# Kernel optimization log

Measured on AMD Instinct MI355X. Metric: run time of the kernel, lower is better.

The kernel has to match this reference:

```python
import jax, jax.numpy as jnp
import numpy as np

H, DH = 8, 32          # heads, per-head dim
C = H * DH             # channels = 256
N = 20000              # nodes
E = 160000             # edges per relation
L = 4                  # layers
R = 2                  # edge types


def setup_inputs() -> dict:
    key = jax.random.key(0)
    ks = jax.random.split(key, 8)
    return {
        "x": jax.random.normal(ks[0], (N, C), jnp.float32),
        "ei0": jax.random.randint(ks[1], (2, E), 0, N, jnp.int32),
        "ei1": jax.random.randint(ks[2], (2, E), 0, N, jnp.int32),
        "kqv_w": jax.random.normal(ks[3], (L, C, 3 * C), jnp.float32) * 0.05,
        "kqv_b": jnp.zeros((L, 3 * C), jnp.float32),
        "out_w": jax.random.normal(ks[4], (L, C, C), jnp.float32) * 0.05,
        "out_b": jnp.zeros((L, C), jnp.float32),
        "skip": jnp.ones((L,), jnp.float32),
        "krel": jax.random.normal(ks[5], (L, R, H, DH, DH), jnp.float32) * 0.1,
        "vrel": jax.random.normal(ks[6], (L, R, H, DH, DH), jnp.float32) * 0.1,
        "prel": jnp.ones((L, R, H), jnp.float32),
        "ln_g": jnp.ones((L - 1, C), jnp.float32),
        "ln_b": jnp.zeros((L - 1, C), jnp.float32),
    }


def _segment_softmax(logits, seg, n):
    m = jax.ops.segment_max(logits, seg, num_segments=n)
    m = jnp.where(jnp.isfinite(m), m, 0.0)  # empty segments -> avoid -inf
    e = jnp.exp(logits - m[seg])
    s = jax.ops.segment_sum(e, seg, num_segments=n)
    return e / jnp.maximum(s[seg], 1e-16)


def _hgt_conv(x, edge_list, kqv_w, kqv_b, out_w, out_b, skip, krel, vrel, prel):
    n = x.shape[0]
    kqv = x @ kqv_w + kqv_b                       # [N, 3C]
    k, q, v = jnp.split(kqv, 3, axis=1)
    k = k.reshape(n, H, DH)
    q = q.reshape(n, H, DH)
    v = v.reshape(n, H, DH)
    logits, msgs, dsts = [], [], []
    for r, ei in enumerate(edge_list):            # loop over fixed small relation set
        src, dst = ei[0], ei[1]
        k_e = jnp.einsum('ehd,hdf->ehf', k[src], krel[r])   # relation-specific keys
        v_e = jnp.einsum('ehd,hdf->ehf', v[src], vrel[r])   # relation-specific values
        a = (q[dst] * k_e).sum(-1) * prel[r] / np.sqrt(DH)  # [E, H]
        logits.append(a)
        msgs.append(v_e)
        dsts.append(dst)
    logits = jnp.concatenate(logits, 0)
    msgs = jnp.concatenate(msgs, 0)
    dst = jnp.concatenate(dsts, 0)
    # softmax per destination node over ALL incoming edge types jointly (PyG HGTConv)
    alpha = _segment_softmax(logits, dst, n)      # [Etot, H]
    agg = jax.ops.segment_sum(msgs * alpha[:, :, None], dst, num_segments=n)
    agg = agg.reshape(n, C)
    a_out = jax.nn.gelu(agg, approximate=False) @ out_w + out_b
    s = jax.nn.sigmoid(skip)                      # skip applies: out dim == in dim
    return s * a_out + (1.0 - s) * x


def _layer_norm(h, g, b, eps=1e-5):
    mu = h.mean(-1, keepdims=True)
    var = ((h - mu) ** 2).mean(-1, keepdims=True)
    return (h - mu) * jax.lax.rsqrt(var + eps) * g + b


def reference(x, ei0, ei1, kqv_w, kqv_b, out_w, out_b, skip, krel, vrel, prel, ln_g, ln_b):
    edge_list = [ei0, ei1]
    h = x
    for i in range(L):
        h = _hgt_conv(h, edge_list, kqv_w[i], kqv_b[i], out_w[i], out_b[i],
                      skip[i], krel[i], vrel[i], prel[i])
        if i < L - 1:
            h = jax.nn.relu(h)
            h = _layer_norm(h, ln_g[i], ln_b[i])
            # dropout: identity in eval mode (p irrelevant at inference)
    return h
```

## Files before the change

kernel.cpp:

```cpp
#include <hip/hip_runtime.h>
#include <math.h>

#define NN 20000
#define NPAD 20096
#define CC 256
#define HH 8
#define EE 160000
#define TE 320000
#define KVSTRIDE 512
#define APAN ((size_t)NPAD*32)
#define BPAN 40960
#define OPAN 8192

typedef unsigned short u16;
typedef unsigned char u8;
typedef __attribute__((ext_vector_type(8))) short bf16x8;
typedef __attribute__((ext_vector_type(4))) float f32x4;
typedef __attribute__((ext_vector_type(2))) float f32x2;

__device__ __forceinline__ float gelu_exact(float x){
    return 0.5f*x*(1.0f+erff(x*0.7071067811865476f));
}
__device__ __forceinline__ u16 f2bf(float f){
    unsigned u = __float_as_uint(f);
    unsigned r = (u + 0x7fffu + ((u >> 16) & 1u)) >> 16;
    return (u16)r;
}
__device__ __forceinline__ float bf2f(u16 s){
    return __uint_as_float(((unsigned)s) << 16);
}
__device__ __forceinline__ void dec8(uint4 u, float* f){
    f[0]=__uint_as_float(u.x<<16); f[1]=__uint_as_float(u.x&0xffff0000u);
    f[2]=__uint_as_float(u.y<<16); f[3]=__uint_as_float(u.y&0xffff0000u);
    f[4]=__uint_as_float(u.z<<16); f[5]=__uint_as_float(u.z&0xffff0000u);
    f[6]=__uint_as_float(u.w<<16); f[7]=__uint_as_float(u.w&0xffff0000u);
}
__device__ __forceinline__ void dec8_fp8(uint2 u, float* f){
    f32x2 a = __builtin_amdgcn_cvt_pk_f32_fp8(u.x, false);
    f32x2 b = __builtin_amdgcn_cvt_pk_f32_fp8(u.x, true);
    f32x2 c = __builtin_amdgcn_cvt_pk_f32_fp8(u.y, false);
    f32x2 d = __builtin_amdgcn_cvt_pk_f32_fp8(u.y, true);
    f[0]=a.x; f[1]=a.y; f[2]=b.x; f[3]=b.y;
    f[4]=c.x; f[5]=c.y; f[6]=d.x; f[7]=d.y;
}
__device__ __forceinline__ uint2 enc8_fp8(const float* f){
    int t0 = __builtin_amdgcn_cvt_pk_fp8_f32(f[0], f[1], 0, false);
    t0     = __builtin_amdgcn_cvt_pk_fp8_f32(f[2], f[3], t0, true);
    int t1 = __builtin_amdgcn_cvt_pk_fp8_f32(f[4], f[5], 0, false);
    t1     = __builtin_amdgcn_cvt_pk_fp8_f32(f[6], f[7], t1, true);
    uint2 r; r.x = (unsigned)t0; r.y = (unsigned)t1;
    return r;
}
__device__ __forceinline__ float dot8(const float* a, const float* b){
    return a[0]*b[0]+a[1]*b[1]+a[2]*b[2]+a[3]*b[3]
          +a[4]*b[4]+a[5]*b[5]+a[6]*b[6]+a[7]*b[7];
}
__device__ __forceinline__ void gload_lds16(const u16* gsrc, u16* lds_dst){
    __builtin_amdgcn_global_load_lds((const __attribute__((address_space(1))) unsigned int*)gsrc,
                                     (__attribute__((address_space(3))) unsigned int*)lds_dst,
                                     16, 0, 0);
}

__global__ void hist_k(const int* __restrict__ ei0, const int* __restrict__ ei1,
                       int* __restrict__ cnt){
    int e = blockIdx.x*256 + threadIdx.x;
    if (e < TE){
        int dst = (e < EE) ? ei0[EE + e] : ei1[EE + (e - EE)];
        atomicAdd(&cnt[dst], 1);
    }
}
__global__ void scan_block_k(const int* __restrict__ cnt, int* __restrict__ incl,
                             int* __restrict__ bsum){
    __shared__ int tmp[256];
    int tid = threadIdx.x;
    int i = blockIdx.x*256 + tid;
    int v = (i < NN) ? cnt[i] : 0;
    tmp[tid] = v;
    __syncthreads();
    for (int d=1; d<256; d<<=1){
        int t = (tid>=d) ? tmp[tid-d] : 0;
        __syncthreads();
        tmp[tid] += t;
        __syncthreads();
    }
    if (i < NN) incl[i] = tmp[tid];
    if (tid == 255) bsum[blockIdx.x] = tmp[255];
}
__global__ void scan_bsum_k(int* bsum, int nb){
    __shared__ int tmp[128];
    int tid = threadIdx.x;
    int v = (tid < nb) ? bsum[tid] : 0;
    tmp[tid] = v;
    __syncthreads();
    for (int d=1; d<128; d<<=1){
        int t = (tid>=d) ? tmp[tid-d] : 0;
        __syncthreads();
        tmp[tid] += t;
        __syncthreads();
    }
    if (tid < nb) bsum[tid] = tmp[tid] - v;
}
__global__ void finalize_rowptr_k(const int* __restrict__ cnt, const int* __restrict__ incl,
                                  const int* __restrict__ bsum, int* __restrict__ row_ptr){
    int i = blockIdx.x*256 + threadIdx.x;
    if (i < NN) row_ptr[i] = incl[i] - cnt[i] + bsum[blockIdx.x];
    if (i == NN) row_ptr[NN] = TE;
}
__global__ void scatter_k(const int* __restrict__ ei0, const int* __restrict__ ei1,
                          const int* __restrict__ row_ptr, int* __restrict__ cursor,
                          int* __restrict__ epk){
    int e = blockIdx.x*256 + threadIdx.x;
    if (e < TE){
        int src, dst, rel;
        if (e < EE){ src = ei0[e]; dst = ei0[EE+e]; rel = 0; }
        else { int ee=e-EE; src = ei1[ee]; dst = ei1[EE+ee]; rel = 1; }
        int pos = atomicAdd(&cursor[dst], 1);
        epk[row_ptr[dst] + pos] = rel*NN + src;
    }
}

__global__ void prep_k(const float* __restrict__ kqv_w, const float* __restrict__ kqv_b,
                       const float* __restrict__ krel, const float* __restrict__ vrel,
                       const float* __restrict__ prel, const float* __restrict__ out_w,
                       const float* __restrict__ x,
                       u16* __restrict__ Wt, u16* __restrict__ xbf, u16* __restrict__ Wto,
                       float* __restrict__ bias5, float* __restrict__ sc5,
                       int* __restrict__ cnt, int* __restrict__ cursor){
    int b = blockIdx.x;
    if (b < 5120){
        int idx = b*256 + threadIdx.x;
        int k = idx & 255;
        int n = (idx >> 8) % 1280;
        int l = idx / (1280*256);
        const float* W = kqv_w + (size_t)l*196608;
        float val;
        if (n < 256){
            val = W[k*768 + 256 + n];
        } else {
            int g = (n-256) >> 8;
            int r = g & 1, isv = g >> 1;
            int c = (n-256) & 255;
            int h = c >> 5, f = c & 31;
            const float* Rm = (isv ? vrel : krel) + ((size_t)l*2 + r)*8192 + h*1024;
            int base = isv ? 512 : 0;
            float a = 0.f;
            #pragma unroll 8
            for (int d=0; d<32; ++d)
                a += W[k*768 + base + h*32 + d] * Rm[d*32 + f];
            val = a;
        }
        Wt[(size_t)l*327680 + (size_t)(k>>5)*BPAN + n*32 + (k&31)] = f2bf(val);
    } else if (b < 7620){
        int idx = (b-5120)*256 + threadIdx.x;
        int e = idx*8;
        int row = e >> 8, col = e & 255;
        const float4* xp = (const float4*)x;
        float4 a = xp[(size_t)idx*2], bb = xp[(size_t)idx*2+1];
        uint4 o;
        o.x = (unsigned)f2bf(a.x) | ((unsigned)f2bf(a.y)<<16);
        o.y = (unsigned)f2bf(a.z) | ((unsigned)f2bf(a.w)<<16);
        o.z = (unsigned)f2bf(bb.x) | ((unsigned)f2bf(bb.y)<<16);
        o.w = (unsigned)f2bf(bb.z) | ((unsigned)f2bf(bb.w)<<16);
        *(uint4*)&xbf[(size_t)(col>>5)*APAN + (size_t)row*32 + (col&31)] = o;
    } else if (b < 8644){
        int idx = (b-7620)*256 + threadIdx.x;
        int k = idx & 255;
        int n = (idx >> 8) & 255;
        int l = idx >> 16;
        Wto[(size_t)l*65536 + (size_t)(k>>5)*OPAN + n*32 + (k&31)] =
            f2bf(out_w[(size_t)l*65536 + k*256 + n]);
    } else if (b < 8664){
        int idx = (b-8644)*256 + threadIdx.x;
        if (idx >= 4*1280) return;
        int n = idx % 1280, l = idx / 1280;
        const float* B = kqv_b + l*768;
        float val, scl = 1.f;
        if (n < 256) val = B[256+n];
        else {
            int g = (n-256) >> 8;
            int r = g & 1, isv = g >> 1;
            int c = (n-256) & 255;
            int h = c >> 5, f = c & 31;
            const float* Rm = (isv ? vrel : krel) + ((size_t)l*2 + r)*8192 + h*1024;
            int base = isv ? 512 : 0;
            float a = 0.f;
            for (int d=0; d<32; ++d) a += B[base + h*32 + d] * Rm[d*32 + f];
            val = a;
            if (!isv) scl = prel[l*16 + r*8 + h] * 0.17677669529663687f;
        }
        bias5[idx] = val;
        sc5[idx] = scl;
    } else {
        int idx = (b-8664)*256 + threadIdx.x;
        int4 z; z.x = 0; z.y = 0; z.z = 0; z.w = 0;
        if (idx < 5000)       ((int4*)cnt)[idx] = z;
        else if (idx < 10000) ((int4*)cursor)[idx-5000] = z;
    }
}

__global__ __launch_bounds__(256) void gemm5_k(const u16* __restrict__ A,
        const u16* __restrict__ Wt, const float* __restrict__ biasp,
        const float* __restrict__ sc5p,
        u16* __restrict__ qb, u8* __restrict__ kvb){
    int L = blockIdx.x;
    int xcd = L & 7;
    int t = L >> 3;
    int ytile = xcd*20 + t/10;
    int xtile = t % 10;
    if (ytile >= 157) return;
    int col0 = xtile * 128;
    int row0 = ytile * 128;

    __shared__ __align__(16) char smem[33792];
    u16* As = (u16*)smem;
    u16* Bs = (u16*)(smem + 16384);
    float* Cs = (float*)smem;
    int tid = threadIdx.x;
    int w = tid >> 6, lane = tid & 63;
    int wm = w & 1, wn = w >> 1;
    f32x4 acc[4][4];
    #pragma unroll
    for (int i=0;i<4;++i)
        #pragma unroll
        for (int j=0;j<4;++j) acc[i][j] = (f32x4){0.f,0.f,0.f,0.f};

    int lm = lane & 15, quad = lane >> 4;
    int kq0 = quad ^ (lm & 3);
    int aoff = (wm*64 + lm)*32 + kq0*8;
    int boff = (wn*64 + lm)*32 + kq0*8;

    for (int kk = 0; kk < 4; ++kk){
        #pragma unroll
        for (int hf = 0; hf < 2; ++hf){
            int pan = kk*2 + hf;
            #pragma unroll
            for (int it = 0; it < 2; ++it){
                int s = w*128 + it*64 + lane;
                int row = s >> 2, q0 = s & 3;
                int kq = q0 ^ (row & 3);
                gload_lds16(&A [(size_t)pan*APAN + (size_t)(row0+row)*32 + kq*8],
                            &As[(size_t)(hf*4096) + (size_t)(w*128 + it*64)*8]);
                gload_lds16(&Wt[(size_t)pan*BPAN + (size_t)(col0+row)*32 + kq*8],
                            &Bs[(size_t)(hf*4096) + (size_t)(w*128 + it*64)*8]);
            }
        }
        __syncthreads();
        #pragma unroll
        for (int hf = 0; hf < 2; ++hf){
            bf16x8 af[4], bfr[4];
            #pragma unroll
            for (int mi=0; mi<4; ++mi) af[mi]  = *(bf16x8*)&As[hf*4096 + aoff + mi*512];
            #pragma unroll
            for (int ni=0; ni<4; ++ni) bfr[ni] = *(bf16x8*)&Bs[hf*4096 + boff + ni*512];
            #pragma unroll
            for (int mi=0; mi<4; ++mi)
                #pragma unroll
                for (int ni=0; ni<4; ++ni)
                    acc[mi][ni] = __builtin_amdgcn_mfma_f32_16x16x32_bf16(af[mi], bfr[ni], acc[mi][ni], 0,0,0);
        }
        __syncthreads();
    }

    int bufi = col0 >> 8;
    int cbase = col0 & 255;
    float bvv[4], scv[4];
    #pragma unroll
    for (int ni=0; ni<4; ++ni){
        bvv[ni] = biasp[col0 + wn*64 + ni*16 + lm];
        scv[ni] = sc5p [col0 + wn*64 + ni*16 + lm];
    }

    int rowl_s = tid >> 3;
    int col8   = tid & 7;
    int gcb    = (col8 >> 2)*64 + (col8 & 3)*8;

    #pragma unroll
    for (int p=0; p<2; ++p){
        if (p) __syncthreads();
        #pragma unroll
        for (int nj=0; nj<2; ++nj){
            int ni = p*2 + nj;
            int lcol = wn*32 + nj*16 + lm;
            #pragma unroll
            for (int mi=0; mi<4; ++mi){
                #pragma unroll
                for (int t2=0; t2<4; ++t2){
                    int lr = wm*64 + mi*16 + quad*4 + t2;
                    Cs[lr*66 + lcol] = (acc[mi][ni][t2] + bvv[ni]) * scv[ni];
                }
            }
        }
        __syncthreads();
        int cw = cbase + gcb + p*32;
        #pragma unroll
        for (int it=0; it<4; ++it){
            int rl = rowl_s + it*32;
            int r = row0 + rl;
            if (r < NN){
                const float* src = &Cs[rl*66 + col8*8];
                float cf[8];
                *(float4*)&cf[0] = *(const float4*)&src[0];
                *(float4*)&cf[4] = *(const float4*)&src[4];
                if (bufi == 0){
                    uint4 o;
                    o.x = (unsigned)f2bf(cf[0]) | ((unsigned)f2bf(cf[1])<<16);
                    o.y = (unsigned)f2bf(cf[2]) | ((unsigned)f2bf(cf[3])<<16);
                    o.z = (unsigned)f2bf(cf[4]) | ((unsigned)f2bf(cf[5])<<16);
                    o.w = (unsigned)f2bf(cf[6]) | ((unsigned)f2bf(cf[7])<<16);
                    *(uint4*)&qb[(size_t)r*256 + cw] = o;
                } else if (bufi <= 2){
                    int rel = bufi - 1;
                    uint2 o = enc8_fp8(cf);
                    *(uint2*)&kvb[(size_t)(rel*NN + r)*KVSTRIDE + cw] = o;
                } else {
                    int rel = bufi - 3;
                    uint2 o = enc8_fp8(cf);
                    *(uint2*)&kvb[(size_t)(rel*NN + r)*KVSTRIDE + 256 + cw] = o;
                }
            }
        }
    }
}

__global__ __launch_bounds__(256) void attn_k(const u16* __restrict__ qb,
        const u8* __restrict__ kvb,
        const int* __restrict__ row_ptr, const int* __restrict__ epk,
        u16* __restrict__ A2){
    int wv = threadIdx.x >> 6, lane = threadIdx.x & 63;
    int node = blockIdx.x*4 + wv;
    int l32 = lane & 31;
    int half = lane >> 5;
    int start = row_ptr[node], end = row_ptr[node+1];
    float qf[8];
    {
        uint4 qr = *(const uint4*)&qb[(size_t)node*256 + l32*8];
        dec8(qr, qf);
    }
    float m = -1e30f, s = 0.f;
    float acc[8] = {0.f,0.f,0.f,0.f,0.f,0.f,0.f,0.f};

    int i0 = start + half;
    uint2 k0={0,0}, k1={0,0}, v0={0,0}, v1={0,0};
    if (i0 < end){
        const u8* row = &kvb[(size_t)epk[i0]*KVSTRIDE];
        k0 = *(const uint2*)(row + l32*8);
        v0 = *(const uint2*)(row + 256 + l32*8);
    }
    if (i0 + 2 < end){
        const u8* row = &kvb[(size_t)epk[i0+2]*KVSTRIDE];
        k1 = *(const uint2*)(row + l32*8);
        v1 = *(const uint2*)(row + 256 + l32*8);
    }
    int pk = (i0 + 4 < end) ? epk[i0+4] : 0;

    for (int i = i0; i < end; i += 2){
        uint2 kc = k0, vc = v0;
        k0 = k1; v0 = v1;
        if (i + 4 < end){
            const u8* row = &kvb[(size_t)pk*KVSTRIDE];
            k1 = *(const uint2*)(row + l32*8);
            v1 = *(const uint2*)(row + 256 + l32*8);
        }
        if (i + 6 < end) pk = epk[i+6];
        float kv[8];
        dec8_fp8(kc, kv);
        float p = dot8(qf, kv);
        p += __shfl_xor(p, 1);
        p += __shfl_xor(p, 2);
        float mo = m;
        m = fmaxf(m, p);
        float sc = __expf(mo - m);
        float pe = __expf(p - m);
        s = s*sc + pe;
        float vv[8];
        dec8_fp8(vc, vv);
        #pragma unroll
        for (int j=0;j<8;++j) acc[j] = acc[j]*sc + pe*vv[j];
    }
    float mO = __shfl_xor(m, 32);
    float mA = fmaxf(m, mO);
    float eS = __expf(m - mA);
    float sh = s * eS;
    float sA = sh + __shfl_xor(sh, 32);
    float rs = 1.f / fmaxf(sA, 1e-16f);
    float oA[8];
    #pragma unroll
    for (int j=0;j<8;++j){
        float a = acc[j] * eS;
        oA[j] = a + __shfl_xor(a, 32);
    }
    if (half == 0){
        u16 o[8];
        #pragma unroll
        for (int j=0;j<8;++j) o[j] = f2bf(gelu_exact(oA[j]*rs));
        uint4 ov;
        ov.x = (unsigned)o[0] | ((unsigned)o[1]<<16);
        ov.y = (unsigned)o[2] | ((unsigned)o[3]<<16);
        ov.z = (unsigned)o[4] | ((unsigned)o[5]<<16);
        ov.w = (unsigned)o[6] | ((unsigned)o[7]<<16);
        int c0 = l32*8;
        *(uint4*)&A2[(size_t)(c0>>5)*APAN + (size_t)node*32 + (c0&31)] = ov;
    }
}

__global__ __launch_bounds__(256) void gemmOln_k(const u16* __restrict__ A,
        const u16* __restrict__ Wt, const float* __restrict__ bias,
        const float* __restrict__ h_in, const float* __restrict__ skip_l,
        const float* __restrict__ g, const float* __restrict__ b,
        float* __restrict__ h_out, u16* __restrict__ hbf){
    __shared__ __align__(16) char smem[36864];
    u16* As = (u16*)smem;
    u16* Bs = (u16*)(smem + 4096);
    float* part_s = (float*)smem;
    float* part_q = part_s + 32*66;
    float* mu_s   = part_q + 32*66;
    float* rstd_s = mu_s + 32;
    int tid = threadIdx.x;
    int w = tid >> 6, lane = tid & 63;
    int row0 = blockIdx.x * 32;
    f32x4 acc[2][4];
    #pragma unroll
    for (int i=0;i<2;++i)
        #pragma unroll
        for (int j=0;j<4;++j) acc[i][j] = (f32x4){0.f,0.f,0.f,0.f};

    int lm = lane & 15, quad = lane >> 4;
    int kq0 = quad ^ (lm & 3);
    int aoff = lm*32 + kq0*8;
    int boff = (w*64 + lm)*32 + kq0*8;

    for (int kk2 = 0; kk2 < 4; ++kk2){
        {
            int s = tid;
            int hf = s >> 7;
            int s7 = s & 127;
            int row = s7 >> 2, q0 = s7 & 3;
            int kq = q0 ^ (row & 3);
            gload_lds16(&A[(size_t)(kk2*2+hf)*APAN + (size_t)(row0+row)*32 + kq*8],
                        &As[(size_t)(w*64)*8]);
        }
        #pragma unroll
        for (int it = 0; it < 8; ++it){
            int s = it*256 + tid;
            int hf = s >> 10;
            int s10 = s & 1023;
            int row = s10 >> 2, q0 = s10 & 3;
            int kq = q0 ^ (row & 3);
            gload_lds16(&Wt[(size_t)(kk2*2+hf)*OPAN + (size_t)row*32 + kq*8],
                        &Bs[(size_t)(it*256 + w*64)*8]);
        }
        __syncthreads();
        #pragma unroll
        for (int hf = 0; hf < 2; ++hf){
            bf16x8 af[2], bfr[4];
            #pragma unroll
            for (int mi=0; mi<2; ++mi) af[mi]  = *(bf16x8*)&As[hf*1024 + aoff + mi*512];
            #pragma unroll
            for (int ni=0; ni<4; ++ni) bfr[ni] = *(bf16x8*)&Bs[hf*8192 + boff + ni*512];
            #pragma unroll
            for (int mi=0; mi<2; ++mi)
                #pragma unroll
                for (int ni=0; ni<4; ++ni)
                    acc[mi][ni] = __builtin_amdgcn_mfma_f32_16x16x32_bf16(af[mi], bfr[ni], acc[mi][ni], 0,0,0);
        }
        __syncthreads();
    }

    float sskip = 1.f/(1.f+__expf(-skip_l[0]));
    float osk = 1.f - sskip;
    float bv[4], gv[4], bbv[4];
    #pragma unroll
    for (int ni=0; ni<4; ++ni){
        int colg = w*64 + ni*16 + lm;
        bv[ni]  = bias[colg];
        gv[ni]  = g[colg];
        bbv[ni] = b[colg];
    }
    #pragma unroll
    for (int mi=0; mi<2; ++mi){
        #pragma unroll
        for (int t=0; t<4; ++t){
            int lr = mi*16 + quad*4 + t;
            int r = row0 + lr;
            float ps = 0.f, pq = 0.f;
            #pragma unroll
            for (int ni=0; ni<4; ++ni){
                int colg = w*64 + ni*16 + lm;
                float hv = h_in[(size_t)r*256 + colg];
                float val = sskip*(acc[mi][ni][t] + bv[ni]) + osk*hv;
                val = fmaxf(val, 0.f);
                acc[mi][ni][t] = val;
                ps += val; pq += val*val;
            }
            part_s[lr*66 + w*16 + lm] = ps;
            part_q[lr*66 + w*16 + lm] = pq;
        }
    }
    __syncthreads();
    if (tid < 32){
        float S = 0.f, Q = 0.f;
        #pragma unroll 8
        for (int t2=0; t2<64; ++t2){
            S += part_s[tid*66 + t2];
            Q += part_q[tid*66 + t2];
        }
        float mu = S * (1.f/256.f);
        float var = Q * (1.f/256.f) - mu*mu;
        mu_s[tid] = mu;
        rstd_s[tid] = rsqrtf(var + 1e-5f);
    }
    __syncthreads();
    #pragma unroll
    for (int mi=0; mi<2; ++mi){
        #pragma unroll
        for (int t=0; t<4; ++t){
            int lr = mi*16 + quad*4 + t;
            int r = row0 + lr;
            float mu = mu_s[lr], rstd = rstd_s[lr];
            #pragma unroll
            for (int ni=0; ni<4; ++ni){
                int colg = w*64 + ni*16 + lm;
                float o = (acc[mi][ni][t] - mu)*rstd*gv[ni] + bbv[ni];
                h_out[(size_t)r*256 + colg] = o;
                hbf[(size_t)(colg>>5)*APAN + (size_t)r*32 + (colg&31)] = f2bf(o);
            }
        }
    }
}

__global__ __launch_bounds__(256) void gemmO_k(const u16* __restrict__ A,
        const u16* __restrict__ Wt, const float* __restrict__ bias,
        const float* __restrict__ h_in, const float* __restrict__ skip_l,
        float* __restrict__ outp){
    __shared__ u16 As[2048];
    __shared__ u16 Bs[4096];
    int tid = threadIdx.x;
    int w = tid >> 6, lane = tid & 63;
    int row0 = blockIdx.x * 64;
    int col0 = blockIdx.y * 128;
    int wm = w & 1, wn = w >> 1;
    f32x4 acc[2][4];
    #pragma unroll
    for (int i=0;i<2;++i)
        #pragma unroll
        for (int j=0;j<4;++j) acc[i][j] = (f32x4){0.f,0.f,0.f,0.f};

    int lm = lane & 15, quad = lane >> 4;
    int kq0 = quad ^ (lm & 3);
    int aoff = (wm*32 + lm)*32 + kq0*8;
    int boff = (wn*64 + lm)*32 + kq0*8;

    for (int kk = 0; kk < 8; ++kk){
        {
            int s = tid;
            int row = s >> 2, q0 = s & 3;
            int kq = q0 ^ (row & 3);
            gload_lds16(&A[(size_t)kk*APAN + (size_t)(row0+row)*32 + kq*8],
                        &As[(size_t)(w*64)*8]);
        }
        #pragma unroll
        for (int it = 0; it < 2; ++it){
            int s = it*256 + tid;
            int row = s >> 2, q0 = s & 3;
            int kq = q0 ^ (row & 3);
            gload_lds16(&Wt[(size_t)kk*OPAN + (size_t)(col0+row)*32 + kq*8],
                        &Bs[(size_t)(it*256 + w*64)*8]);
        }
        __syncthreads();
        bf16x8 af[2], bfr[4];
        #pragma unroll
        for (int mi=0; mi<2; ++mi) af[mi]  = *(bf16x8*)&As[aoff + mi*512];
        #pragma unroll
        for (int ni=0; ni<4; ++ni) bfr[ni] = *(bf16x8*)&Bs[boff + ni*512];
        #pragma unroll
        for (int mi=0; mi<2; ++mi)
            #pragma unroll
            for (int ni=0; ni<4; ++ni)
                acc[mi][ni] = __builtin_amdgcn_mfma_f32_16x16x32_bf16(af[mi], bfr[ni], acc[mi][ni], 0,0,0);
        __syncthreads();
    }
    float s = 1.f/(1.f+expf(-skip_l[0]));
    float os = 1.f - s;
    #pragma unroll
    for (int ni=0; ni<4; ++ni){
        int colg = col0 + wn*64 + ni*16 + lm;
        float bv = bias[colg];
        #pragma unroll
        for (int mi=0; mi<2; ++mi){
            #pragma unroll
            for (int t=0; t<4; ++t){
                int r = row0 + wm*32 + mi*16 + quad*4 + t;
                if (r < NN)
                    outp[(size_t)r*256 + colg] =
                        s*(acc[mi][ni][t] + bv) + os*h_in[(size_t)r*256 + colg];
            }
        }
    }
}

extern "C" void kernel_launch(void* const* d_in, const int* in_sizes, int n_in,
                              void* d_out, int out_size, void* d_ws, size_t ws_size,
                              hipStream_t stream){
    (void)in_sizes; (void)n_in; (void)out_size; (void)ws_size;
    const float* x     = (const float*)d_in[0];
    const int*   ei0   = (const int*)d_in[1];
    const int*   ei1   = (const int*)d_in[2];
    const float* kqv_w = (const float*)d_in[3];
    const float* kqv_b = (const float*)d_in[4];
    const float* out_w = (const float*)d_in[5];
    const float* out_b = (const float*)d_in[6];
    const float* skip  = (const float*)d_in[7];
    const float* krel  = (const float*)d_in[8];
    const float* vrel  = (const float*)d_in[9];
    const float* prel  = (const float*)d_in[10];
    const float* ln_g  = (const float*)d_in[11];
    const float* ln_b  = (const float*)d_in[12];
    float* outp = (float*)d_out;

    char* wp = (char*)d_ws;
    auto alloc = [&](size_t bytes)->void*{
        void* p = wp; wp += (bytes + 255) & ~(size_t)255; return p;
    };
    float* hA    = (float*)alloc((size_t)NN*CC*4);
    float* hB    = (float*)alloc((size_t)NN*CC*4);
    u16*   xbf   = (u16*)alloc((size_t)NPAD*CC*2);
    u16*   hbf   = (u16*)alloc((size_t)NPAD*CC*2);
    u16*   A2    = (u16*)alloc((size_t)NPAD*CC*2);
    u16*   qb    = (u16*)alloc((size_t)NN*CC*2);
    u8*    kvb   = (u8*)alloc((size_t)2*NN*KVSTRIDE);
    u16*   Wt5   = (u16*)alloc((size_t)4*1280*256*2);
    u16*   Wto   = (u16*)alloc((size_t)4*256*256*2);
    float* bias5 = (float*)alloc((size_t)4*1280*4);
    float* sc5   = (float*)alloc((size_t)4*1280*4);
    int* cnt     = (int*)alloc((size_t)NN*4);
    int* cursor  = (int*)alloc((size_t)NN*4);
    int* incl    = (int*)alloc((size_t)NN*4);
    int* row_ptr = (int*)alloc((size_t)(NN+1)*4);
    int* bsum    = (int*)alloc(128*4);
    int* epk     = (int*)alloc((size_t)TE*4);

    prep_k<<<8704,256,0,stream>>>(kqv_w, kqv_b, krel, vrel, prel, out_w, x,
                                  Wt5, xbf, Wto, bias5, sc5, cnt, cursor);

    hist_k<<<1250,256,0,stream>>>(ei0, ei1, cnt);
    scan_block_k<<<79,256,0,stream>>>(cnt, incl, bsum);
    scan_bsum_k<<<1,128,0,stream>>>(bsum, 79);
    finalize_rowptr_k<<<79,256,0,stream>>>(cnt, incl, bsum, row_ptr);
    scatter_k<<<1250,256,0,stream>>>(ei0, ei1, row_ptr, cursor, epk);

    const float* h_in = x;
    const u16*   Ain  = xbf;
    float* houts[4] = {hA, hB, hA, outp};
    for (int l=0; l<4; ++l){
        gemm5_k<<<1600,256,0,stream>>>(Ain, Wt5 + (size_t)l*327680,
                bias5 + l*1280, sc5 + l*1280, qb, kvb);
        attn_k<<<5000,256,0,stream>>>(qb, kvb, row_ptr, epk, A2);
        if (l < 3){
            gemmOln_k<<<625,256,0,stream>>>(A2, Wto + (size_t)l*65536,
                    out_b + l*256, h_in, skip + l, ln_g + l*256, ln_b + l*256,
                    houts[l], hbf);
        } else {
            gemmO_k<<<dim3(313,2),256,0,stream>>>(A2, Wto + (size_t)l*65536,
                    out_b + l*256, h_in, skip + l, outp);
        }
        h_in = houts[l];
        Ain = hbf;
    }
}
```

Measured before the change: 380.9 us.

## Interleave K/V rows, vectorize attention, restructure weight prep, fold bsum scan

The K and V fp8 values for each source row are interleaved so each lane fetches a single 16-byte load per edge instead of two 8-byte loads, and prefetch depth rises to three edges. The attention math moves to packed float2 operations. Weight prep now computes the relation-folded K/V projections with one block per (layer, group, head), caching the 32x32 relation matrix in LDS, which cuts the prep grid. The separate block-sum scan kernel is dropped and each finalize block sums the earlier block totals itself with a wave reduction.

```diff
diff --git a/kernel.cpp b/kernel.cpp
--- a/kernel.cpp
+++ b/kernel.cpp
@@ -26,23 +26,6 @@
     unsigned r = (u + 0x7fffu + ((u >> 16) & 1u)) >> 16;
     return (u16)r;
 }
-__device__ __forceinline__ float bf2f(u16 s){
-    return __uint_as_float(((unsigned)s) << 16);
-}
-__device__ __forceinline__ void dec8(uint4 u, float* f){
-    f[0]=__uint_as_float(u.x<<16); f[1]=__uint_as_float(u.x&0xffff0000u);
-    f[2]=__uint_as_float(u.y<<16); f[3]=__uint_as_float(u.y&0xffff0000u);
-    f[4]=__uint_as_float(u.z<<16); f[5]=__uint_as_float(u.z&0xffff0000u);
-    f[6]=__uint_as_float(u.w<<16); f[7]=__uint_as_float(u.w&0xffff0000u);
-}
-__device__ __forceinline__ void dec8_fp8(uint2 u, float* f){
-    f32x2 a = __builtin_amdgcn_cvt_pk_f32_fp8(u.x, false);
-    f32x2 b = __builtin_amdgcn_cvt_pk_f32_fp8(u.x, true);
-    f32x2 c = __builtin_amdgcn_cvt_pk_f32_fp8(u.y, false);
-    f32x2 d = __builtin_amdgcn_cvt_pk_f32_fp8(u.y, true);
-    f[0]=a.x; f[1]=a.y; f[2]=b.x; f[3]=b.y;
-    f[4]=c.x; f[5]=c.y; f[6]=d.x; f[7]=d.y;
-}
 __device__ __forceinline__ uint2 enc8_fp8(const float* f){
     int t0 = __builtin_amdgcn_cvt_pk_fp8_f32(f[0], f[1], 0, false);
     t0     = __builtin_amdgcn_cvt_pk_fp8_f32(f[2], f[3], t0, true);
@@ -50,10 +33,6 @@
     t1     = __builtin_amdgcn_cvt_pk_fp8_f32(f[6], f[7], t1, true);
     uint2 r; r.x = (unsigned)t0; r.y = (unsigned)t1;
     return r;
-}
-__device__ __forceinline__ float dot8(const float* a, const float* b){
-    return a[0]*b[0]+a[1]*b[1]+a[2]*b[2]+a[3]*b[3]
-          +a[4]*b[4]+a[5]*b[5]+a[6]*b[6]+a[7]*b[7];
 }
 __device__ __forceinline__ void gload_lds16(const u16* gsrc, u16* lds_dst){
     __builtin_amdgcn_global_load_lds((const __attribute__((address_space(1))) unsigned int*)gsrc,
@@ -86,24 +65,19 @@
     if (i < NN) incl[i] = tmp[tid];
     if (tid == 255) bsum[blockIdx.x] = tmp[255];
 }
-__global__ void scan_bsum_k(int* bsum, int nb){
-    __shared__ int tmp[128];
-    int tid = threadIdx.x;
-    int v = (tid < nb) ? bsum[tid] : 0;
-    tmp[tid] = v;
-    __syncthreads();
-    for (int d=1; d<128; d<<=1){
-        int t = (tid>=d) ? tmp[tid-d] : 0;
-        __syncthreads();
-        tmp[tid] += t;
-        __syncthreads();
-    }
-    if (tid < nb) bsum[tid] = tmp[tid] - v;
-}
 __global__ void finalize_rowptr_k(const int* __restrict__ cnt, const int* __restrict__ incl,
                                   const int* __restrict__ bsum, int* __restrict__ row_ptr){
-    int i = blockIdx.x*256 + threadIdx.x;
-    if (i < NN) row_ptr[i] = incl[i] - cnt[i] + bsum[blockIdx.x];
+    __shared__ int wsum[4];
+    int tid = threadIdx.x;
+    int bid = blockIdx.x;
+    int v = (tid < bid) ? bsum[tid] : 0;
+    #pragma unroll
+    for (int d=1; d<64; d<<=1) v += __shfl_xor(v, d);
+    if ((tid & 63) == 0) wsum[tid >> 6] = v;
+    __syncthreads();
+    int bpre = wsum[0] + wsum[1] + wsum[2] + wsum[3];
+    int i = bid*256 + tid;
+    if (i < NN) row_ptr[i] = incl[i] - cnt[i] + bpre;
     if (i == NN) row_ptr[NN] = TE;
 }
 __global__ void scatter_k(const int* __restrict__ ei0, const int* __restrict__ ei1,
@@ -127,31 +101,53 @@
                        float* __restrict__ bias5, float* __restrict__ sc5,
                        int* __restrict__ cnt, int* __restrict__ cursor){
     int b = blockIdx.x;
-    if (b < 5120){
-        int idx = b*256 + threadIdx.x;
-        int k = idx & 255;
-        int n = (idx >> 8) % 1280;
-        int l = idx / (1280*256);
+    int tid = threadIdx.x;
+    if (b < 1024){
+        int l = b >> 8, n = b & 255;
+        int k = tid;
         const float* W = kqv_w + (size_t)l*196608;
-        float val;
-        if (n < 256){
-            val = W[k*768 + 256 + n];
-        } else {
-            int g = (n-256) >> 8;
-            int r = g & 1, isv = g >> 1;
-            int c = (n-256) & 255;
-            int h = c >> 5, f = c & 31;
-            const float* Rm = (isv ? vrel : krel) + ((size_t)l*2 + r)*8192 + h*1024;
-            int base = isv ? 512 : 0;
-            float a = 0.f;
-            #pragma unroll 8
-            for (int d=0; d<32; ++d)
-                a += W[k*768 + base + h*32 + d] * Rm[d*32 + f];
-            val = a;
-        }
+        float val = W[k*768 + 256 + n];
         Wt[(size_t)l*327680 + (size_t)(k>>5)*BPAN + n*32 + (k&31)] = f2bf(val);
-    } else if (b < 7620){
-        int idx = (b-5120)*256 + threadIdx.x;
+    } else if (b < 1152){
+        int b2 = b - 1024;
+        int l = b2 >> 5;
+        int g = (b2 >> 3) & 3;
+        int h = b2 & 7;
+        int r = g & 1, isv = g >> 1;
+        __shared__ float Rs[32*36];
+        const float* Rm = (isv ? vrel : krel) + ((size_t)l*2 + r)*8192 + h*1024;
+        #pragma unroll
+        for (int j=0; j<4; ++j){
+            int idx = tid + 256*j;
+            Rs[(idx>>5)*36 + (idx&31)] = Rm[idx];
+        }
+        __syncthreads();
+        int base = isv ? 512 : 0;
+        const float* W = kqv_w + (size_t)l*196608 + (size_t)tid*768 + base + h*32;
+        float w[32];
+        #pragma unroll 8
+        for (int d=0; d<32; ++d) w[d] = W[d];
+        f32x4 acc4[8];
+        #pragma unroll
+        for (int fb=0; fb<8; ++fb) acc4[fb] = (f32x4){0.f,0.f,0.f,0.f};
+        for (int d=0; d<32; ++d){
+            float wd = w[d];
+            f32x4 wv = (f32x4){wd,wd,wd,wd};
+            #pragma unroll
+            for (int fb=0; fb<8; ++fb){
+                f32x4 rv = *(const f32x4*)&Rs[d*36 + fb*4];
+                acc4[fb] += wv * rv;
+            }
+        }
+        int nb = 256 + g*256 + h*32;
+        size_t wbase = (size_t)l*327680 + (size_t)(tid>>5)*BPAN + (size_t)(tid&31);
+        #pragma unroll
+        for (int fb=0; fb<8; ++fb)
+            #pragma unroll
+            for (int e=0; e<4; ++e)
+                Wt[wbase + (size_t)(nb + fb*4 + e)*32] = f2bf(acc4[fb][e]);
+    } else if (b < 3652){
+        int idx = (b-1152)*256 + tid;
         int e = idx*8;
         int row = e >> 8, col = e & 255;
         const float4* xp = (const float4*)x;
@@ -162,16 +158,15 @@
         o.z = (unsigned)f2bf(bb.x) | ((unsigned)f2bf(bb.y)<<16);
         o.w = (unsigned)f2bf(bb.z) | ((unsigned)f2bf(bb.w)<<16);
         *(uint4*)&xbf[(size_t)(col>>5)*APAN + (size_t)row*32 + (col&31)] = o;
-    } else if (b < 8644){
-        int idx = (b-7620)*256 + threadIdx.x;
+    } else if (b < 4676){
+        int idx = (b-3652)*256 + tid;
         int k = idx & 255;
         int n = (idx >> 8) & 255;
         int l = idx >> 16;
         Wto[(size_t)l*65536 + (size_t)(k>>5)*OPAN + n*32 + (k&31)] =
             f2bf(out_w[(size_t)l*65536 + k*256 + n]);
-    } else if (b < 8664){
-        int idx = (b-8644)*256 + threadIdx.x;
-        if (idx >= 4*1280) return;
+    } else if (b < 4696){
+        int idx = (b-4676)*256 + tid;
         int n = idx % 1280, l = idx / 1280;
         const float* B = kqv_b + l*768;
         float val, scl = 1.f;
@@ -191,7 +186,7 @@
         bias5[idx] = val;
         sc5[idx] = scl;
     } else {
-        int idx = (b-8664)*256 + threadIdx.x;
+        int idx = (b-4696)*256 + tid;
         int4 z; z.x = 0; z.y = 0; z.z = 0; z.w = 0;
         if (idx < 5000)       ((int4*)cnt)[idx] = z;
         else if (idx < 10000) ((int4*)cursor)[idx-5000] = z;
@@ -311,11 +306,11 @@
                 } else if (bufi <= 2){
                     int rel = bufi - 1;
                     uint2 o = enc8_fp8(cf);
-                    *(uint2*)&kvb[(size_t)(rel*NN + r)*KVSTRIDE + cw] = o;
+                    *(uint2*)&kvb[(size_t)(rel*NN + r)*KVSTRIDE + cw*2] = o;
                 } else {
                     int rel = bufi - 3;
                     uint2 o = enc8_fp8(cf);
-                    *(uint2*)&kvb[(size_t)(rel*NN + r)*KVSTRIDE + 256 + cw] = o;
+                    *(uint2*)&kvb[(size_t)(rel*NN + r)*KVSTRIDE + cw*2 + 8] = o;
                 }
             }
         }
@@ -331,40 +326,37 @@
     int l32 = lane & 31;
     int half = lane >> 5;
     int start = row_ptr[node], end = row_ptr[node+1];
-    float qf[8];
+    f32x2 qf[4];
     {
         uint4 qr = *(const uint4*)&qb[(size_t)node*256 + l32*8];
-        dec8(qr, qf);
+        qf[0] = (f32x2){__uint_as_float(qr.x<<16), __uint_as_float(qr.x&0xffff0000u)};
+        qf[1] = (f32x2){__uint_as_float(qr.y<<16), __uint_as_float(qr.y&0xffff0000u)};
+        qf[2] = (f32x2){__uint_as_float(qr.z<<16), __uint_as_float(qr.z&0xffff0000u)};
+        qf[3] = (f32x2){__uint_as_float(qr.w<<16), __uint_as_float(qr.w&0xffff0000u)};
     }
     float m = -1e30f, s = 0.f;
-    float acc[8] = {0.f,0.f,0.f,0.f,0.f,0.f,0.f,0.f};
+    f32x2 acc[4];
+    #pragma unroll
+    for (int j=0;j<4;++j) acc[j] = (f32x2){0.f,0.f};
 
     int i0 = start + half;
-    uint2 k0={0,0}, k1={0,0}, v0={0,0}, v1={0,0};
-    if (i0 < end){
-        const u8* row = &kvb[(size_t)epk[i0]*KVSTRIDE];
-        k0 = *(const uint2*)(row + l32*8);
-        v0 = *(const uint2*)(row + 256 + l32*8);
-    }
-    if (i0 + 2 < end){
-        const u8* row = &kvb[(size_t)epk[i0+2]*KVSTRIDE];
-        k1 = *(const uint2*)(row + l32*8);
-        v1 = *(const uint2*)(row + 256 + l32*8);
-    }
-    int pk = (i0 + 4 < end) ? epk[i0+4] : 0;
+    uint4 c0={0,0,0,0}, c1={0,0,0,0}, c2={0,0,0,0};
+    if (i0     < end) c0 = *(const uint4*)&kvb[(size_t)epk[i0  ]*KVSTRIDE + l32*16];
+    if (i0 + 2 < end) c1 = *(const uint4*)&kvb[(size_t)epk[i0+2]*KVSTRIDE + l32*16];
+    if (i0 + 4 < end) c2 = *(const uint4*)&kvb[(size_t)epk[i0+4]*KVSTRIDE + l32*16];
+    int pk = (i0 + 6 < end) ? epk[i0+6] : 0;
 
     for (int i = i0; i < end; i += 2){
-        uint2 kc = k0, vc = v0;
-        k0 = k1; v0 = v1;
-        if (i + 4 < end){
-            const u8* row = &kvb[(size_t)pk*KVSTRIDE];
-            k1 = *(const uint2*)(row + l32*8);
-            v1 = *(const uint2*)(row + 256 + l32*8);
-        }
-        if (i + 6 < end) pk = epk[i+6];
-        float kv[8];
-        dec8_fp8(kc, kv);
-        float p = dot8(qf, kv);
+        uint4 cc = c0; c0 = c1; c1 = c2;
+        if (i + 6 < end)
+            c2 = *(const uint4*)&kvb[(size_t)pk*KVSTRIDE + l32*16];
+        if (i + 8 < end) pk = epk[i+8];
+        f32x2 kf0 = __builtin_amdgcn_cvt_pk_f32_fp8(cc.x, false);
+        f32x2 kf1 = __builtin_amdgcn_cvt_pk_f32_fp8(cc.x, true);
+        f32x2 kf2 = __builtin_amdgcn_cvt_pk_f32_fp8(cc.y, false);
+        f32x2 kf3 = __builtin_amdgcn_cvt_pk_f32_fp8(cc.y, true);
+        f32x2 p2 = qf[0]*kf0 + qf[1]*kf1 + qf[2]*kf2 + qf[3]*kf3;
+        float p = p2.x + p2.y;
         p += __shfl_xor(p, 1);
         p += __shfl_xor(p, 2);
         float mo = m;
@@ -372,10 +364,15 @@
         float sc = __expf(mo - m);
         float pe = __expf(p - m);
         s = s*sc + pe;
-        float vv[8];
-        dec8_fp8(vc, vv);
-        #pragma unroll
-        for (int j=0;j<8;++j) acc[j] = acc[j]*sc + pe*vv[j];
+        f32x2 vf0 = __builtin_amdgcn_cvt_pk_f32_fp8(cc.z, false);
+        f32x2 vf1 = __builtin_amdgcn_cvt_pk_f32_fp8(cc.z, true);
+        f32x2 vf2 = __builtin_amdgcn_cvt_pk_f32_fp8(cc.w, false);
+        f32x2 vf3 = __builtin_amdgcn_cvt_pk_f32_fp8(cc.w, true);
+        f32x2 sc2 = (f32x2){sc,sc}, pe2 = (f32x2){pe,pe};
+        acc[0] = acc[0]*sc2 + pe2*vf0;
+        acc[1] = acc[1]*sc2 + pe2*vf1;
+        acc[2] = acc[2]*sc2 + pe2*vf2;
+        acc[3] = acc[3]*sc2 + pe2*vf3;
     }
     float mO = __shfl_xor(m, 32);
     float mA = fmaxf(m, mO);
@@ -385,9 +382,10 @@
     float rs = 1.f / fmaxf(sA, 1e-16f);
     float oA[8];
     #pragma unroll
-    for (int j=0;j<8;++j){
-        float a = acc[j] * eS;
-        oA[j] = a + __shfl_xor(a, 32);
+    for (int j=0;j<4;++j){
+        f32x2 a = acc[j] * (f32x2){eS,eS};
+        oA[2*j]   = a.x + __shfl_xor(a.x, 32);
+        oA[2*j+1] = a.y + __shfl_xor(a.y, 32);
     }
     if (half == 0){
         u16 o[8];
@@ -398,8 +396,8 @@
         ov.y = (unsigned)o[2] | ((unsigned)o[3]<<16);
         ov.z = (unsigned)o[4] | ((unsigned)o[5]<<16);
         ov.w = (unsigned)o[6] | ((unsigned)o[7]<<16);
-        int c0 = l32*8;
-        *(uint4*)&A2[(size_t)(c0>>5)*APAN + (size_t)node*32 + (c0&31)] = ov;
+        int c0b = l32*8;
+        *(uint4*)&A2[(size_t)(c0b>>5)*APAN + (size_t)node*32 + (c0b&31)] = ov;
     }
 }
 
@@ -639,12 +637,11 @@
     int* bsum    = (int*)alloc(128*4);
     int* epk     = (int*)alloc((size_t)TE*4);
 
-    prep_k<<<8704,256,0,stream>>>(kqv_w, kqv_b, krel, vrel, prel, out_w, x,
+    prep_k<<<4736,256,0,stream>>>(kqv_w, kqv_b, krel, vrel, prel, out_w, x,
                                   Wt5, xbf, Wto, bias5, sc5, cnt, cursor);
 
     hist_k<<<1250,256,0,stream>>>(ei0, ei1, cnt);
     scan_block_k<<<79,256,0,stream>>>(cnt, incl, bsum);
-    scan_bsum_k<<<1,128,0,stream>>>(bsum, 79);
     finalize_rowptr_k<<<79,256,0,stream>>>(cnt, incl, bsum, row_ptr);
     scatter_k<<<1250,256,0,stream>>>(ei0, ei1, row_ptr, cursor, epk);
 
```

After: 357.5 us. 6.1% less time.
